# Kernel optimization log

Hardware: AMD Instinct MI355X
Metric: run time of the kernel (lower is better)

The kernel has to match this reference:

```python
import jax, jax.numpy as jnp
import numpy as np

T, A = 2048, 64          # n_thread, n_agents
RAWOB, N_TP, N_GP = 120, 5, 2
E = N_TP * N_GP          # number of sub-nets (type x group placeholder)
D = RAWOB + N_TP + 1     # augmented obs dim fed to each Net
H = 128                  # hidden width of each sub-net MLP
N_ACTION = 16


def setup_inputs() -> dict:
    key = jax.random.key(0)
    ks = jax.random.split(key, 12)
    s1 = 1.0 / np.sqrt(D)
    s2 = 1.0 / np.sqrt(H)
    return {
        "obs": jax.random.normal(ks[0], (T, A, RAWOB), dtype=jnp.float32),
        "hete_pick": jax.random.randint(ks[1], (T, A), 0, E),
        "hete_type": jax.random.randint(ks[2], (T, A), 0, N_TP),
        "gp_sel_summary": jax.random.randint(ks[3], (T, N_TP), 0, N_GP),
        # per-expert actor MLP params [E, ...]
        "W1": jax.random.normal(ks[4], (E, D, H), dtype=jnp.float32) * s1,
        "b1": jnp.zeros((E, H), dtype=jnp.float32),
        "W2": jax.random.normal(ks[5], (E, H, N_ACTION), dtype=jnp.float32) * s2,
        "b2": jnp.zeros((E, N_ACTION), dtype=jnp.float32),
        # central critic params
        "Wc1": jax.random.normal(ks[6], (D, H), dtype=jnp.float32) * s1,
        "bc1": jnp.zeros((H,), dtype=jnp.float32),
        "Wc2": jax.random.normal(ks[7], (H, 1), dtype=jnp.float32) * s2,
        "bc2": jnp.zeros((1,), dtype=jnp.float32),
    }


def _augment_obs(obs, hete_type, gp_sel_summary):
    # obs <- cat(obs, hete_type, gp_sel_summary with -1 scattered at own type idx)
    t, a, _ = obs.shape
    n_tp = gp_sel_summary.shape[1]
    gp = jnp.broadcast_to(gp_sel_summary[:, None, :].astype(obs.dtype), (t, a, n_tp))
    oh = jax.nn.one_hot(hete_type, n_tp, dtype=obs.dtype)
    gp_obs = gp * (1.0 - oh) - oh  # scatter -1 at index hete_type
    return jnp.concatenate([obs, hete_type[..., None].astype(obs.dtype), gp_obs], axis=-1)


def reference(obs, hete_pick, hete_type, gp_sel_summary,
              W1, b1, W2, b2, Wc1, bc1, Wc2, bc2):
    t, a, _ = obs.shape
    x = _augment_obs(obs, hete_type, gp_sel_summary)          # [T, A, D]
    xf = x.reshape(t * a, -1)                                  # [N, D]
    pick = hete_pick.reshape(t * a)                            # [N]
    n_exp = W1.shape[0]
    # dispatch: each token routed to exactly one sub-net; dense compute + masked combine
    logits = jnp.zeros((t * a, W2.shape[-1]), dtype=obs.dtype)
    for e in range(n_exp):  # small fixed expert loop
        y = jax.nn.relu(xf @ W1[e] + b1[e]) @ W2[e] + b2[e]    # [N, n_action]
        logits = jnp.where((pick == e)[:, None], y, logits)
    logits = logits.reshape(t, a, -1)
    # central critic on all tokens
    value = (jax.nn.relu(xf @ Wc1 + bc1) @ Wc2 + bc2).reshape(t, a, 1)
    return logits, value
```

## Files before the change

kernel.cpp:

```cpp
#include <hip/hip_runtime.h>
#include <hip/hip_bf16.h>

#define T_DIM   2048
#define A_DIM   64
#define N_TOK   (T_DIM * A_DIM)
#define RAWOB   120
#define N_TP    5
#define E_EXP   10
#define D_DIM   126
#define DP      128
#define H_DIM   128
#define N_ACT   16
#define CAP     14336
#define BTOK    256
#define MAXC    (CAP / BTOK)
#define LOGITS_SZ (N_TOK * N_ACT)

typedef __bf16 bh8 __attribute__((ext_vector_type(8)));
typedef ushort u16x8 __attribute__((ext_vector_type(8)));
typedef ushort u16x4 __attribute__((ext_vector_type(4)));
typedef short  s16x4 __attribute__((ext_vector_type(4)));
typedef float  f32x4 __attribute__((ext_vector_type(4)));

__device__ __forceinline__ f32x4 mfma16(bh8 a, bh8 b, f32x4 c) {
    return __builtin_amdgcn_mfma_f32_16x16x32_bf16(a, b, c, 0, 0, 0);
}
__device__ __forceinline__ f32x4 mfma16k16(s16x4 a, s16x4 b, f32x4 c) {
    return __builtin_amdgcn_mfma_f32_16x16x16bf16_1k(a, b, c, 0, 0, 0);
}

__device__ __forceinline__ ushort f2bf(float f) {
    unsigned x = __builtin_bit_cast(unsigned, f);
    unsigned r = (x + 0x7fffu + ((x >> 16) & 1u)) >> 16;
    return (ushort)r;
}

#define W1P_N (E_EXP * H_DIM * DP)
#define W2P_N (E_EXP * N_ACT * H_DIM)
#define WC1P_N (DP * DP)

#define LDS_W2  16384
#define LDS_WC1 18432
#define LDS_TOT 34816

#define PB_BLOCKS 156

__global__ __launch_bounds__(256) void prep_bucket_kernel(
    const float* __restrict__ W1, const float* __restrict__ W2,
    const float* __restrict__ Wc1, const float* __restrict__ b1,
    const float* __restrict__ bc1, const int* __restrict__ pick,
    int* __restrict__ counts, int* __restrict__ order,
    ushort* __restrict__ W1p, ushort* __restrict__ W2p, ushort* __restrict__ Wc1p)
{
    int bx = blockIdx.x, tid = threadIdx.x;
    if (bx < 44) {
        __shared__ ushort st[32][130];
        const float* src;
        const float* bias;
        ushort* dstbase;
        int kt;
        if (bx < 40) {
            int e = bx >> 2;
            kt = bx & 3;
            src = W1 + (e * D_DIM + kt * 32) * H_DIM;
            bias = b1 + e * H_DIM;
            dstbase = W1p + e * (H_DIM * DP);
        } else {
            kt = bx - 40;
            src = Wc1 + kt * 32 * H_DIM;
            bias = bc1;
            dstbase = Wc1p;
        }
        int dmax = D_DIM - kt * 32;
#pragma unroll
        for (int p = 0; p < 16; ++p) {
            int idx = p * 256 + tid;
            int dd = idx >> 7, n = idx & 127;
            float v;
            if (dd < dmax)                    v = src[dd * H_DIM + n];
            else if (kt == 3 && dd == 30)     v = bias[n];
            else                              v = 0.f;
            st[dd][n] = f2bf(v);
        }
        __syncthreads();
#pragma unroll
        for (int p = 0; p < 16; ++p) {
            int idx = p * 256 + tid;
            int dd = idx >> 7, n = idx & 127;
            dstbase[((n >> 4) * 4 + kt) * 512 + ((dd >> 3) * 16 + (n & 15)) * 8 + (dd & 7)]
                = st[dd][n];
        }
    } else if (bx < 124) {
        int i = (bx - 44) * 256 + tid;
        int e   = i >> 11;
        int rem = i & 2047;
        int kk  = rem >> 8;
        int idx = rem & 255;
        int l = idx >> 2, j = idx & 3;
        int lq = l >> 4, lm = l & 15;
        W2p[i] = f2bf(W2[(e * H_DIM + kk * 16 + lq * 4 + j) * N_ACT + lm]);
    } else {
        __shared__ int lc[E_EXP], lb[E_EXP];
        if (tid < E_EXP) lc[tid] = 0;
        __syncthreads();
        int base = (bx - 124) * 4096;
        int ev[16], loc[16];
#pragma unroll
        for (int it = 0; it < 16; ++it) {
            ev[it] = pick[base + it * 256 + tid];
            loc[it] = atomicAdd(&lc[ev[it]], 1);
        }
        __syncthreads();
        if (tid < E_EXP) lb[tid] = atomicAdd(&counts[tid * 16], lc[tid]);
        __syncthreads();
#pragma unroll
        for (int it = 0; it < 16; ++it) {
            int e = ev[it];
            int pos = lb[e] + loc[it];
            if (pos < CAP) order[e * CAP + pos] = base + it * 256 + tid;
        }
    }
}

__global__ __launch_bounds__(512, 6) void moe_kernel(
    const float* __restrict__ obs, const int* __restrict__ hete_type,
    const int* __restrict__ gp_sel,
    const float* __restrict__ b2, const float* __restrict__ bc2,
    const int* __restrict__ order,
    const ushort* __restrict__ W1p, const ushort* __restrict__ W2p,
    const ushort* __restrict__ Wc1p, const float* __restrict__ Wc2,
    float* __restrict__ out)
{
    __shared__ __align__(16) ushort wlds[LDS_TOT];

    const int bx = blockIdx.x;
    const int e = bx % E_EXP;
    const int c = bx / E_EXP;
    const int tid = threadIdx.x;
    const int w = tid >> 6;
    const int base = c * BTOK + w * 32;
    const int l = tid & 63;
    const int lm = l & 15;
    const int lq = l >> 4;

    const int* ord_e = order + e * CAP;

    int sraw[2];
    sraw[0] = ord_e[base + lm];
    sraw[1] = ord_e[base + 16 + lm];

    {
        const u16x8* s1 = (const u16x8*)(const void*)(W1p + e * (H_DIM * DP));
        u16x8* d1 = (u16x8*)(void*)wlds;
#pragma unroll
        for (int p = 0; p < 4; ++p) d1[p * 512 + tid] = s1[p * 512 + tid];
        const u16x8* sc = (const u16x8*)(const void*)Wc1p;
        u16x8* dc = (u16x8*)(void*)(wlds + LDS_WC1);
#pragma unroll
        for (int p = 0; p < 4; ++p) dc[p * 512 + tid] = sc[p * 512 + tid];
        if (tid < 256)
            ((u16x8*)(void*)(wlds + LDS_W2))[tid] =
                ((const u16x8*)(const void*)(W2p + e * 2048))[tid];
    }

    bh8 a[2][4];
    int tokm[2];
#pragma unroll
    for (int mt = 0; mt < 2; ++mt) {
        const int tok = sraw[mt] < 0 ? 0 : sraw[mt];
        tokm[mt] = tok;
        const float* orow = obs + tok * RAWOB;
#pragma unroll
        for (int kt = 0; kt < 3; ++kt) {
            const float* p = orow + kt * 32 + lq * 8;
            float4 u0 = *(const float4*)(const void*)p;
            float4 u1 = *(const float4*)(const void*)(p + 4);
            u16x8 t;
            t[0] = f2bf(u0.x); t[1] = f2bf(u0.y); t[2] = f2bf(u0.z); t[3] = f2bf(u0.w);
            t[4] = f2bf(u1.x); t[5] = f2bf(u1.y); t[6] = f2bf(u1.z); t[7] = f2bf(u1.w);
            a[mt][kt] = __builtin_bit_cast(bh8, t);
        }
        u16x8 t;
        if (lq < 3) {
            const float* p = orow + 96 + lq * 8;
            float4 u0 = *(const float4*)(const void*)p;
            float4 u1 = *(const float4*)(const void*)(p + 4);
            t[0] = f2bf(u0.x); t[1] = f2bf(u0.y); t[2] = f2bf(u0.z); t[3] = f2bf(u0.w);
            t[4] = f2bf(u1.x); t[5] = f2bf(u1.y); t[6] = f2bf(u1.z); t[7] = f2bf(u1.w);
        } else {
            int ht = hete_type[tok];
            int tt = tok >> 6;
            t[0] = f2bf((float)ht);
#pragma unroll
            for (int q = 0; q < N_TP; ++q) {
                float g = (q == ht) ? -1.0f : (float)gp_sel[tt * N_TP + q];
                t[1 + q] = f2bf(g);
            }
            t[6] = (ushort)0x3F80;
            t[7] = 0;
        }
        a[mt][3] = __builtin_bit_cast(bh8, t);
    }

    const float bb  = b2[e * N_ACT + lm];
    const float bcv = bc2[0];

    __syncthreads();

    {
        f32x4 y0 = (f32x4){0.f, 0.f, 0.f, 0.f};
        f32x4 y1 = (f32x4){0.f, 0.f, 0.f, 0.f};
#pragma unroll
        for (int nt = 0; nt < 8; ++nt) {
            f32x4 ae0 = (f32x4){0.f, 0.f, 0.f, 0.f}, ae1 = ae0;
#pragma unroll
            for (int kt = 0; kt < 4; ++kt) {
                bh8 wf = *(const bh8*)(const void*)(wlds + (nt * 4 + kt) * 512 + l * 8);
                ae0 = mfma16(wf, a[0][kt], ae0);
                ae1 = mfma16(wf, a[1][kt], ae1);
            }
            u16x4 hp0, hp1;
#pragma unroll
            for (int r = 0; r < 4; ++r) {
                hp0[r] = f2bf(fmaxf(ae0[r], 0.f));
                hp1[r] = f2bf(fmaxf(ae1[r], 0.f));
            }
            s16x4 w2f = *(const s16x4*)(const void*)(wlds + LDS_W2 + nt * 256 + l * 4);
            y0 = mfma16k16(__builtin_bit_cast(s16x4, hp0), w2f, y0);
            y1 = mfma16k16(__builtin_bit_cast(s16x4, hp1), w2f, y1);
        }
#pragma unroll
        for (int r = 0; r < 4; ++r) {
            int s0 = ord_e[base + lq * 4 + r];
            if (s0 >= 0) out[s0 * N_ACT + lm] = y0[r] + bb;
            int s1 = ord_e[base + 16 + lq * 4 + r];
            if (s1 >= 0) out[s1 * N_ACT + lm] = y1[r] + bb;
        }
    }

    {
        float p0 = 0.f, p1 = 0.f;
#pragma unroll
        for (int nt = 0; nt < 8; ++nt) {
            f32x4 c0 = (f32x4){0.f,0.f,0.f,0.f}, c1 = c0;
#pragma unroll
            for (int kt = 0; kt < 4; ++kt) {
                bh8 wf = *(const bh8*)(const void*)
                         (wlds + LDS_WC1 + (nt * 4 + kt) * 512 + l * 8);
                c0 = mfma16(wf, a[0][kt], c0);
                c1 = mfma16(wf, a[1][kt], c1);
            }
            const float4 wc = *(const float4*)(const void*)(Wc2 + nt * 16 + lq * 4);
            p0 += fmaxf(c0[0], 0.f) * wc.x + fmaxf(c0[1], 0.f) * wc.y
                + fmaxf(c0[2], 0.f) * wc.z + fmaxf(c0[3], 0.f) * wc.w;
            p1 += fmaxf(c1[0], 0.f) * wc.x + fmaxf(c1[1], 0.f) * wc.y
                + fmaxf(c1[2], 0.f) * wc.z + fmaxf(c1[3], 0.f) * wc.w;
        }
        p0 += __shfl_xor(p0, 16, 64); p0 += __shfl_xor(p0, 32, 64);
        p1 += __shfl_xor(p1, 16, 64); p1 += __shfl_xor(p1, 32, 64);
        if (lq == 0) {
            if (sraw[0] >= 0) out[LOGITS_SZ + tokm[0]] = p0 + bcv;
            if (sraw[1] >= 0) out[LOGITS_SZ + tokm[1]] = p1 + bcv;
        }
    }
}

extern "C" void kernel_launch(void* const* d_in, const int* in_sizes, int n_in,
                              void* d_out, int out_size, void* d_ws, size_t ws_size,
                              hipStream_t stream) {
    const float* obs  = (const float*)d_in[0];
    const int*   pick = (const int*)d_in[1];
    const int*   htyp = (const int*)d_in[2];
    const int*   gp   = (const int*)d_in[3];
    const float* W1   = (const float*)d_in[4];
    const float* b1   = (const float*)d_in[5];
    const float* W2   = (const float*)d_in[6];
    const float* b2   = (const float*)d_in[7];
    const float* Wc1  = (const float*)d_in[8];
    const float* bc1  = (const float*)d_in[9];
    const float* Wc2  = (const float*)d_in[10];
    const float* bc2  = (const float*)d_in[11];
    float* out = (float*)d_out;

    int*    counts = (int*)d_ws;
    int*    order  = counts + 160;
    ushort* W1p    = (ushort*)(order + E_EXP * CAP);
    ushort* W2p    = W1p + W1P_N;
    ushort* Wc1p   = W2p + W2P_N;

    hipMemsetAsync(counts, 0, 160 * sizeof(int), stream);
    hipMemsetAsync(order, 0xFF, E_EXP * CAP * sizeof(int), stream);
    prep_bucket_kernel<<<PB_BLOCKS, 256, 0, stream>>>(
        W1, W2, Wc1, b1, bc1, pick, counts, order, W1p, W2p, Wc1p);
    moe_kernel<<<E_EXP * MAXC, 512, 0, stream>>>(
        obs, htyp, gp, b2, bc2, order,
        W1p, W2p, Wc1p, Wc2, out);
}
```

Measured before the change: 139.3 us.

## Pre-gather augmented bf16 activations per expert in prep kernel; read Wc1 from global

```diff
diff --git a/kernel.cpp b/kernel.cpp
--- a/kernel.cpp
+++ b/kernel.cpp
@@ -38,19 +38,22 @@
 #define W1P_N (E_EXP * H_DIM * DP)
 #define W2P_N (E_EXP * N_ACT * H_DIM)
 #define WC1P_N (DP * DP)
+#define XG_N  (E_EXP * CAP * 128)
 
 #define LDS_W2  16384
-#define LDS_WC1 18432
-#define LDS_TOT 34816
-
-#define PB_BLOCKS 156
+#define LDS_TOT 18432
+
+#define PB_BLOCKS 636
 
 __global__ __launch_bounds__(256) void prep_bucket_kernel(
     const float* __restrict__ W1, const float* __restrict__ W2,
     const float* __restrict__ Wc1, const float* __restrict__ b1,
     const float* __restrict__ bc1, const int* __restrict__ pick,
+    const float* __restrict__ obs, const int* __restrict__ hete_type,
+    const int* __restrict__ gp_sel,
     int* __restrict__ counts, int* __restrict__ order,
-    ushort* __restrict__ W1p, ushort* __restrict__ W2p, ushort* __restrict__ Wc1p)
+    ushort* __restrict__ W1p, ushort* __restrict__ W2p, ushort* __restrict__ Wc1p,
+    ushort* __restrict__ xg)
 {
     int bx = blockIdx.x, tid = threadIdx.x;
     if (bx < 44) {
@@ -101,30 +104,58 @@
         W2p[i] = f2bf(W2[(e * H_DIM + kk * 16 + lq * 4 + j) * N_ACT + lm]);
     } else {
         __shared__ int lc[E_EXP], lb[E_EXP];
+        __shared__ int stok[256], sslot[256];
+        const int tok = (bx - 124) * 256 + tid;
         if (tid < E_EXP) lc[tid] = 0;
         __syncthreads();
-        int base = (bx - 124) * 4096;
-        int ev[16], loc[16];
-#pragma unroll
-        for (int it = 0; it < 16; ++it) {
-            ev[it] = pick[base + it * 256 + tid];
-            loc[it] = atomicAdd(&lc[ev[it]], 1);
-        }
+        const int e = pick[tok];
+        const int loc = atomicAdd(&lc[e], 1);
         __syncthreads();
         if (tid < E_EXP) lb[tid] = atomicAdd(&counts[tid * 16], lc[tid]);
         __syncthreads();
-#pragma unroll
-        for (int it = 0; it < 16; ++it) {
-            int e = ev[it];
-            int pos = lb[e] + loc[it];
-            if (pos < CAP) order[e * CAP + pos] = base + it * 256 + tid;
+        const int pos = lb[e] + loc;
+        int s = -1;
+        if (pos < CAP) {
+            s = e * CAP + pos;
+            order[s] = tok;
+        }
+        stok[tid] = tok;
+        sslot[tid] = s;
+        __syncthreads();
+        const int chunk = tid & 15;
+#pragma unroll 4
+        for (int p = 0; p < 16; ++p) {
+            const int ti = p * 16 + (tid >> 4);
+            const int ss = sslot[ti];
+            if (ss < 0) continue;
+            const int tk = stok[ti];
+            ushort* dst = xg + (size_t)ss * 128 + chunk * 8;
+            u16x8 t;
+            if (chunk < 15) {
+                const float* p0 = obs + tk * RAWOB + chunk * 8;
+                float4 u0 = *(const float4*)(const void*)p0;
+                float4 u1 = *(const float4*)(const void*)(p0 + 4);
+                t[0] = f2bf(u0.x); t[1] = f2bf(u0.y); t[2] = f2bf(u0.z); t[3] = f2bf(u0.w);
+                t[4] = f2bf(u1.x); t[5] = f2bf(u1.y); t[6] = f2bf(u1.z); t[7] = f2bf(u1.w);
+            } else {
+                int ht = hete_type[tk];
+                int tt = tk >> 6;
+                t[0] = f2bf((float)ht);
+#pragma unroll
+                for (int q = 0; q < N_TP; ++q) {
+                    float g = (q == ht) ? -1.0f : (float)gp_sel[tt * N_TP + q];
+                    t[1 + q] = f2bf(g);
+                }
+                t[6] = (ushort)0x3F80;
+                t[7] = 0;
+            }
+            *(u16x8*)(void*)dst = t;
         }
     }
 }
 
 __global__ __launch_bounds__(512, 6) void moe_kernel(
-    const float* __restrict__ obs, const int* __restrict__ hete_type,
-    const int* __restrict__ gp_sel,
+    const ushort* __restrict__ xg,
     const float* __restrict__ b2, const float* __restrict__ bc2,
     const int* __restrict__ order,
     const ushort* __restrict__ W1p, const ushort* __restrict__ W2p,
@@ -136,15 +167,17 @@
     const int bx = blockIdx.x;
     const int e = bx % E_EXP;
     const int c = bx / E_EXP;
+    const int start = c * BTOK;
+    const int* ord_e = order + e * CAP;
+    if (ord_e[start] < 0) return;
+
     const int tid = threadIdx.x;
     const int w = tid >> 6;
-    const int base = c * BTOK + w * 32;
+    const int base = start + w * 32;
     const int l = tid & 63;
     const int lm = l & 15;
     const int lq = l >> 4;
 
-    const int* ord_e = order + e * CAP;
-
     int sraw[2];
     sraw[0] = ord_e[base + lm];
     sraw[1] = ord_e[base + 16 + lm];
@@ -154,53 +187,19 @@
         u16x8* d1 = (u16x8*)(void*)wlds;
 #pragma unroll
         for (int p = 0; p < 4; ++p) d1[p * 512 + tid] = s1[p * 512 + tid];
-        const u16x8* sc = (const u16x8*)(const void*)Wc1p;
-        u16x8* dc = (u16x8*)(void*)(wlds + LDS_WC1);
-#pragma unroll
-        for (int p = 0; p < 4; ++p) dc[p * 512 + tid] = sc[p * 512 + tid];
         if (tid < 256)
             ((u16x8*)(void*)(wlds + LDS_W2))[tid] =
                 ((const u16x8*)(const void*)(W2p + e * 2048))[tid];
     }
 
+    const ushort* xbase = xg + (size_t)(e * CAP + base) * 128;
     bh8 a[2][4];
-    int tokm[2];
-#pragma unroll
-    for (int mt = 0; mt < 2; ++mt) {
-        const int tok = sraw[mt] < 0 ? 0 : sraw[mt];
-        tokm[mt] = tok;
-        const float* orow = obs + tok * RAWOB;
-#pragma unroll
-        for (int kt = 0; kt < 3; ++kt) {
-            const float* p = orow + kt * 32 + lq * 8;
-            float4 u0 = *(const float4*)(const void*)p;
-            float4 u1 = *(const float4*)(const void*)(p + 4);
-            u16x8 t;
-            t[0] = f2bf(u0.x); t[1] = f2bf(u0.y); t[2] = f2bf(u0.z); t[3] = f2bf(u0.w);
-            t[4] = f2bf(u1.x); t[5] = f2bf(u1.y); t[6] = f2bf(u1.z); t[7] = f2bf(u1.w);
-            a[mt][kt] = __builtin_bit_cast(bh8, t);
-        }
-        u16x8 t;
-        if (lq < 3) {
-            const float* p = orow + 96 + lq * 8;
-            float4 u0 = *(const float4*)(const void*)p;
-            float4 u1 = *(const float4*)(const void*)(p + 4);
-            t[0] = f2bf(u0.x); t[1] = f2bf(u0.y); t[2] = f2bf(u0.z); t[3] = f2bf(u0.w);
-            t[4] = f2bf(u1.x); t[5] = f2bf(u1.y); t[6] = f2bf(u1.z); t[7] = f2bf(u1.w);
-        } else {
-            int ht = hete_type[tok];
-            int tt = tok >> 6;
-            t[0] = f2bf((float)ht);
-#pragma unroll
-            for (int q = 0; q < N_TP; ++q) {
-                float g = (q == ht) ? -1.0f : (float)gp_sel[tt * N_TP + q];
-                t[1 + q] = f2bf(g);
-            }
-            t[6] = (ushort)0x3F80;
-            t[7] = 0;
-        }
-        a[mt][3] = __builtin_bit_cast(bh8, t);
-    }
+#pragma unroll
+    for (int mt = 0; mt < 2; ++mt)
+#pragma unroll
+        for (int kt = 0; kt < 4; ++kt)
+            a[mt][kt] = *(const bh8*)(const void*)
+                        (xbase + (mt * 16 + lm) * 128 + kt * 32 + lq * 8);
 
     const float bb  = b2[e * N_ACT + lm];
     const float bcv = bc2[0];
@@ -245,8 +244,7 @@
             f32x4 c0 = (f32x4){0.f,0.f,0.f,0.f}, c1 = c0;
 #pragma unroll
             for (int kt = 0; kt < 4; ++kt) {
-                bh8 wf = *(const bh8*)(const void*)
-                         (wlds + LDS_WC1 + (nt * 4 + kt) * 512 + l * 8);
+                bh8 wf = *(const bh8*)(const void*)(Wc1p + (nt * 4 + kt) * 512 + l * 8);
                 c0 = mfma16(wf, a[0][kt], c0);
                 c1 = mfma16(wf, a[1][kt], c1);
             }
@@ -259,8 +257,8 @@
         p0 += __shfl_xor(p0, 16, 64); p0 += __shfl_xor(p0, 32, 64);
         p1 += __shfl_xor(p1, 16, 64); p1 += __shfl_xor(p1, 32, 64);
         if (lq == 0) {
-            if (sraw[0] >= 0) out[LOGITS_SZ + tokm[0]] = p0 + bcv;
-            if (sraw[1] >= 0) out[LOGITS_SZ + tokm[1]] = p1 + bcv;
+            if (sraw[0] >= 0) out[LOGITS_SZ + sraw[0]] = p0 + bcv;
+            if (sraw[1] >= 0) out[LOGITS_SZ + sraw[1]] = p1 + bcv;
         }
     }
 }
@@ -287,12 +285,13 @@
     ushort* W1p    = (ushort*)(order + E_EXP * CAP);
     ushort* W2p    = W1p + W1P_N;
     ushort* Wc1p   = W2p + W2P_N;
+    ushort* xg     = Wc1p + WC1P_N;
 
     hipMemsetAsync(counts, 0, 160 * sizeof(int), stream);
     hipMemsetAsync(order, 0xFF, E_EXP * CAP * sizeof(int), stream);
     prep_bucket_kernel<<<PB_BLOCKS, 256, 0, stream>>>(
-        W1, W2, Wc1, b1, bc1, pick, counts, order, W1p, W2p, Wc1p);
+        W1, W2, Wc1, b1, bc1, pick, obs, htyp, gp,
+        counts, order, W1p, W2p, Wc1p, xg);
     moe_kernel<<<E_EXP * MAXC, 512, 0, stream>>>(
-        obs, htyp, gp, b2, bc2, order,
-        W1p, W2p, Wc1p, Wc2, out);
-}
+        xg, b2, bc2, order, W1p, W2p, Wc1p, Wc2, out);
+}
```

New measurement: 173.3 us. 1.24x slower.
